# Optimization experiments

Measured on AMD Instinct MI355X. Metric: run time of the kernel, lower is better.

The kernel has to match this reference:

```python
import jax, jax.numpy as jnp
import numpy as np

N_NODES = 50000
N_EDGES = 800000
NODE_FEAT = 176
EDGE_FEAT = 4
HIDDEN = 64
LAYERS = 4
LN_EPS = 1e-5


def setup_inputs() -> dict:
    key = jax.random.key(0)
    ks = jax.random.split(key, 20)
    H, H2, Hh = HIDDEN, HIDDEN * 2, HIDDEN // 2
    inp = {
        "x": jax.random.normal(ks[0], (N_NODES, NODE_FEAT), jnp.float32),
        "edge_index": jax.random.randint(ks[1], (2, N_EDGES), 0, N_NODES, jnp.int64),
        "edge_attr": jax.random.normal(ks[2], (N_EDGES, EDGE_FEAT), jnp.float32),
        # input projection
        "in_w": jax.random.normal(ks[3], (NODE_FEAT, H), jnp.float32) * 0.05,
        "in_b": jnp.zeros((H,), jnp.float32),
        # per-layer GINEConv params (stacked over LAYERS)
        "edge_w": jax.random.normal(ks[4], (LAYERS, EDGE_FEAT, H), jnp.float32) * 0.1,
        "edge_b": jnp.zeros((LAYERS, H), jnp.float32),
        "mlp_w1": jax.random.normal(ks[5], (LAYERS, H, H2), jnp.float32) * 0.05,
        "mlp_b1": jnp.zeros((LAYERS, H2), jnp.float32),
        "mlp_w2": jax.random.normal(ks[6], (LAYERS, H2, H), jnp.float32) * 0.05,
        "mlp_b2": jnp.zeros((LAYERS, H), jnp.float32),
        "ln_g": jnp.ones((LAYERS, H), jnp.float32),
        "ln_b": jnp.zeros((LAYERS, H), jnp.float32),
        "reg_w1": jax.random.normal(ks[7], (H, Hh), jnp.float32) * 0.1,
        "reg_b1": jnp.zeros((Hh,), jnp.float32),
        "reg_w2": jax.random.normal(ks[8], (Hh, 1), jnp.float32) * 0.1,
        "reg_b2": jnp.zeros((1,), jnp.float32),
    }
    return inp


def _layernorm(z, g, b):
    mu = jnp.mean(z, axis=-1, keepdims=True)
    var = jnp.mean((z - mu) ** 2, axis=-1, keepdims=True)
    return g * (z - mu) * jax.lax.rsqrt(var + LN_EPS) + b


def reference(x, edge_index, edge_attr, in_w, in_b, edge_w, edge_b,
              mlp_w1, mlp_b1, mlp_w2, mlp_b2, ln_g, ln_b,
              reg_w1, reg_b1, reg_w2, reg_b2):
    src, dst = edge_index[0], edge_index[1]
    h = x @ in_w + in_b  # [N, H]
    for l in range(LAYERS):
        e = edge_attr @ edge_w[l] + edge_b[l]              # [E, H] edge projection
        msg = jax.nn.relu(h[src] + e)                      # gather + relu
        aggr = jax.ops.segment_sum(msg, dst, num_segments=h.shape[0])  # scatter-add
        z = h + aggr                                       # (1+eps)*x_i + aggr, eps=0
        z = jax.nn.relu(z @ mlp_w1[l] + mlp_b1[l]) @ mlp_w2[l] + mlp_b2[l]
        h = jax.nn.relu(_layernorm(z, ln_g[l], ln_b[l]))
    g = jnp.sum(h, axis=0)                                 # global_add_pool, single graph
    out = jax.nn.relu(g @ reg_w1 + reg_b1) @ reg_w2 + reg_b2
    return out.squeeze()
```

## Files before the change

### kernel.cpp

```cpp
#include <hip/hip_runtime.h>

#define N_NODES 50000
#define N_EDGES 800000
#define NODE_FEAT 176
#define HIDDEN 64
#define LN_EPS 1e-5f
#define SCAN_NB 49

typedef short bf16x8 __attribute__((ext_vector_type(8)));
typedef float f32x4 __attribute__((ext_vector_type(4)));

__device__ __forceinline__ unsigned short f2bf(float f) {
    unsigned int u = __float_as_uint(f);
    u += 0x7FFFu + ((u >> 16) & 1u);
    return (unsigned short)(u >> 16);
}
__device__ __forceinline__ int pack2(float lo, float hi) {
    return (int)(((unsigned)f2bf(hi) << 16) | (unsigned)f2bf(lo));
}
__device__ __forceinline__ float bf2f(unsigned short s) {
    return __uint_as_float(((unsigned int)s) << 16);
}
__device__ __forceinline__ float wave_sum64(float v) {
#pragma unroll
    for (int o = 32; o > 0; o >>= 1) v += __shfl_xor(v, o);
    return v;
}
__device__ __forceinline__ float sum16(float v) {
#pragma unroll
    for (int o = 8; o > 0; o >>= 1) v += __shfl_xor(v, o);
    return v;
}

__global__ __launch_bounds__(256) void k_wprep(const float* __restrict__ in_w,
                                               const float* __restrict__ w1,
                                               const float* __restrict__ w2,
                                               unsigned short* __restrict__ fin,
                                               unsigned short* __restrict__ f1,
                                               unsigned short* __restrict__ f2) {
    int t = blockIdx.x * 256 + threadIdx.x;
    if (t < 12288) {
        int e = t;
        int r = e & 7, lane = (e >> 3) & 63, j = (e >> 9) & 3, s = e >> 11;
        int k = s * 32 + ((lane >> 4) << 3) + r;
        int n = (j << 4) + (lane & 15);
        fin[e] = (k < NODE_FEAT) ? f2bf(in_w[k * 64 + n]) : (unsigned short)0;
    } else if (t < 12288 + 32768) {
        int e = t - 12288;
        int L = e >> 13, e2 = e & 8191;
        int r = e2 & 7, lane = (e2 >> 3) & 63, j = (e2 >> 9) & 7, s = (e2 >> 12) & 1;
        int k = s * 32 + ((lane >> 4) << 3) + r;
        int n = (j << 4) + (lane & 15);
        f1[e] = f2bf(w1[L * 8192 + k * 128 + n]);
    } else {
        int e = t - 45056;
        int L = e >> 13, e2 = e & 8191;
        int r = e2 & 7, lane = (e2 >> 3) & 63, j = (e2 >> 9) & 3, s = (e2 >> 11) & 3;
        int k = s * 32 + ((lane >> 4) << 3) + r;
        int n = (j << 4) + (lane & 15);
        f2[e] = f2bf(w2[L * 8192 + k * 64 + n]);
    }
}

__global__ __launch_bounds__(256) void k_inproj_mfma(const float* __restrict__ x,
                                                     const unsigned short* __restrict__ wfrag,
                                                     const float* __restrict__ in_b,
                                                     float* __restrict__ h,
                                                     unsigned short* __restrict__ hb) {
    __shared__ unsigned short lw[12288];
    const int tid = threadIdx.x;
    {
        const bf16x8* src = (const bf16x8*)wfrag;
        bf16x8* dst = (bf16x8*)lw;
        for (int i = tid; i < 1536; i += 256) dst[i] = src[i];
    }
    __syncthreads();
    const int wv = tid >> 6, lane = tid & 63;
    const int lrow = lane & 15, lgrp = lane >> 4;
    float ib[4];
#pragma unroll
    for (int j = 0; j < 4; ++j) ib[j] = in_b[16 * j + lrow];
    const int nwaves = gridDim.x * 4;
    for (int tile = blockIdx.x * 4 + wv; tile < 3125; tile += nwaves) {
        const int m0 = tile * 16;
        f32x4 acc[4];
#pragma unroll
        for (int j = 0; j < 4; ++j) acc[j] = (f32x4){ib[j], ib[j], ib[j], ib[j]};
#pragma unroll
        for (int s = 0; s < 6; ++s) {
            const int kbase = s * 32 + lgrp * 8;
            bf16x8 a;
            if (kbase < NODE_FEAT) {
                const float* p = x + (size_t)(m0 + lrow) * NODE_FEAT + kbase;
                float4 fa = *(const float4*)p;
                float4 fb = *(const float4*)(p + 4);
                a[0] = (short)f2bf(fa.x); a[1] = (short)f2bf(fa.y);
                a[2] = (short)f2bf(fa.z); a[3] = (short)f2bf(fa.w);
                a[4] = (short)f2bf(fb.x); a[5] = (short)f2bf(fb.y);
                a[6] = (short)f2bf(fb.z); a[7] = (short)f2bf(fb.w);
            } else {
                a = (bf16x8){0, 0, 0, 0, 0, 0, 0, 0};
            }
#pragma unroll
            for (int j = 0; j < 4; ++j) {
                bf16x8 b = *(const bf16x8*)&lw[((s * 4 + j) * 64 + lane) * 8];
                acc[j] = __builtin_amdgcn_mfma_f32_16x16x32_bf16(a, b, acc[j], 0, 0, 0);
            }
        }
#pragma unroll
        for (int j = 0; j < 4; ++j) {
            const int col = 16 * j + lrow;
#pragma unroll
            for (int r = 0; r < 4; ++r) {
                const int node = m0 + lgrp * 4 + r;
                float v = acc[j][r];
                h[(size_t)node * 64 + col] = v;
                hb[(size_t)node * 64 + col] = f2bf(v);
            }
        }
    }
}

__global__ __launch_bounds__(256) void k_hist(const int* __restrict__ ei,
                                              int* __restrict__ cnt,
                                              int* __restrict__ erank) {
    int e = blockIdx.x * 256 + threadIdx.x;
    if (e < N_EDGES) erank[e] = atomicAdd(&cnt[ei[N_EDGES + e]], 1);
}

__global__ __launch_bounds__(256) void k_scan_part(const int* __restrict__ cnt,
                                                   int* __restrict__ blksum) {
    const int b = blockIdx.x, t = threadIdx.x;
    const int base = b * 1024 + t * 4;
    int s = 0;
#pragma unroll
    for (int i = 0; i < 4; ++i) {
        int idx = base + i;
        if (idx < N_NODES) s += cnt[idx];
    }
#pragma unroll
    for (int o = 32; o > 0; o >>= 1) s += __shfl_xor(s, o);
    __shared__ int wt[4];
    if ((t & 63) == 0) wt[t >> 6] = s;
    __syncthreads();
    if (t == 0) blksum[b] = wt[0] + wt[1] + wt[2] + wt[3];
}

__global__ __launch_bounds__(64) void k_scan_top(const int* __restrict__ blksum,
                                                 int* __restrict__ blkoff,
                                                 int* __restrict__ row_last) {
    const int t = threadIdx.x;
    int v = (t < SCAN_NB) ? blksum[t] : 0;
    int incl = v;
#pragma unroll
    for (int o = 1; o < 64; o <<= 1) {
        int u = __shfl_up(incl, o);
        if (t >= o) incl += u;
    }
    if (t < SCAN_NB) blkoff[t] = incl - v;
    if (t == 63) row_last[0] = incl;
}

__global__ __launch_bounds__(256) void k_scan_add(const int* __restrict__ cnt,
                                                  const int* __restrict__ blkoff,
                                                  int* __restrict__ row_ptr) {
    const int b = blockIdx.x, t = threadIdx.x;
    const int base = b * 1024 + t * 4;
    int c[4];
    int tsum = 0;
#pragma unroll
    for (int i = 0; i < 4; ++i) {
        int idx = base + i;
        c[i] = (idx < N_NODES) ? cnt[idx] : 0;
        tsum += c[i];
    }
    int incl = tsum;
#pragma unroll
    for (int o = 1; o < 64; o <<= 1) {
        int u = __shfl_up(incl, o);
        if ((t & 63) >= o) incl += u;
    }
    __shared__ int wt[4];
    const int wv = t >> 6;
    if ((t & 63) == 63) wt[wv] = incl;
    __syncthreads();
    int run = blkoff[b] + (incl - tsum);
    for (int w = 0; w < wv; ++w) run += wt[w];
#pragma unroll
    for (int i = 0; i < 4; ++i) {
        int idx = base + i;
        if (idx < N_NODES) row_ptr[idx] = run;
        run += c[i];
    }
}

__global__ __launch_bounds__(256) void k_scatter(const int* __restrict__ ei,
                                                 const float4* __restrict__ ea,
                                                 const int* __restrict__ row_ptr,
                                                 const int* __restrict__ erank,
                                                 int4* __restrict__ rec) {
    int e = blockIdx.x * 256 + threadIdx.x;
    if (e >= N_EDGES) return;
    int d = ei[N_EDGES + e];
    float4 a = ea[e];
    int4 r;
    r.x = pack2(a.x, a.y);
    r.y = pack2(a.z, a.w);
    r.z = ei[e];
    r.w = 0;
    rec[row_ptr[d] + erank[e]] = r;
}

__global__ __launch_bounds__(256) void k_aggr(const float* __restrict__ h_in,
                                              const unsigned short* __restrict__ hb_in,
                                              float* __restrict__ z,
                                              const int* __restrict__ row_ptr,
                                              const int4* __restrict__ rec,
                                              const float* __restrict__ ew,
                                              const float* __restrict__ eb) {
    const int wv = threadIdx.x >> 6, lane = threadIdx.x & 63;
    const int node = blockIdx.x * 4 + wv;
    const float ew0 = ew[0 * 64 + lane], ew1 = ew[1 * 64 + lane];
    const float ew2 = ew[2 * 64 + lane], ew3 = ew[3 * 64 + lane];
    const float ebl = eb[lane];
    const int beg = __builtin_amdgcn_readfirstlane(row_ptr[node]);
    const int end = __builtin_amdgcn_readfirstlane(row_ptr[node + 1]);
    float acc = h_in[(size_t)node * 64 + lane];
    int i = beg;
    for (; i + 7 < end; i += 8) {
        int d0[8], d1[8], sx[8];
#pragma unroll
        for (int t = 0; t < 8; ++t) {
            int4 r = rec[i + t];
            d0[t] = __builtin_amdgcn_readfirstlane(r.x);
            d1[t] = __builtin_amdgcn_readfirstlane(r.y);
            sx[t] = __builtin_amdgcn_readfirstlane(r.z);
        }
        float gg[8];
#pragma unroll
        for (int t = 0; t < 8; ++t) {
            const unsigned short* __restrict__ p = hb_in + ((size_t)sx[t] << 6);
            gg[t] = bf2f(p[lane]);
        }
#pragma unroll
        for (int t = 0; t < 8; ++t) {
            float a0 = __uint_as_float((unsigned)d0[t] << 16);
            float a1 = __uint_as_float((unsigned)d0[t] & 0xffff0000u);
            float a2 = __uint_as_float((unsigned)d1[t] << 16);
            float a3 = __uint_as_float((unsigned)d1[t] & 0xffff0000u);
            float v = fmaf(a0, ew0, fmaf(a1, ew1, fmaf(a2, ew2, fmaf(a3, ew3, ebl))));
            acc += fmaxf(v + gg[t], 0.0f);
        }
    }
    for (; i < end; ++i) {
        int4 r = rec[i];
        int d0 = __builtin_amdgcn_readfirstlane(r.x);
        int d1 = __builtin_amdgcn_readfirstlane(r.y);
        int sx = __builtin_amdgcn_readfirstlane(r.z);
        const unsigned short* __restrict__ p = hb_in + ((size_t)sx << 6);
        float g0 = bf2f(p[lane]);
        float a0 = __uint_as_float((unsigned)d0 << 16);
        float a1 = __uint_as_float((unsigned)d0 & 0xffff0000u);
        float a2 = __uint_as_float((unsigned)d1 << 16);
        float a3 = __uint_as_float((unsigned)d1 & 0xffff0000u);
        float v = fmaf(a0, ew0, fmaf(a1, ew1, fmaf(a2, ew2, fmaf(a3, ew3, ebl))));
        acc += fmaxf(v + g0, 0.0f);
    }
    z[(size_t)node * 64 + lane] = acc;
}

__global__ __launch_bounds__(256) void k_mlp_mfma(float* __restrict__ z,
                                                  unsigned short* __restrict__ hb_out,
                                                  const unsigned short* __restrict__ f1,
                                                  const unsigned short* __restrict__ f2,
                                                  const float* __restrict__ b1,
                                                  const float* __restrict__ b2,
                                                  const float* __restrict__ lng,
                                                  const float* __restrict__ lnb) {
    __shared__ unsigned short w1f[8192];
    __shared__ unsigned short w2f[8192];
    __shared__ unsigned short z1s[4][2048];
    const int tid = threadIdx.x;
    {
        const bf16x8* s1 = (const bf16x8*)f1;
        const bf16x8* s2 = (const bf16x8*)f2;
        bf16x8* d1 = (bf16x8*)w1f;
        bf16x8* d2 = (bf16x8*)w2f;
        for (int i = tid; i < 1024; i += 256) { d1[i] = s1[i]; d2[i] = s2[i]; }
    }
    __syncthreads();
    const int wv = tid >> 6, lane = tid & 63;
    const int lrow = lane & 15, lgrp = lane >> 4;
    unsigned short* zs = z1s[wv];
    float bb1[8], bb2[4], g4[4], be4[4];
#pragma unroll
    for (int j = 0; j < 8; ++j) bb1[j] = b1[16 * j + lrow];
#pragma unroll
    for (int j = 0; j < 4; ++j) {
        bb2[j] = b2[16 * j + lrow];
        g4[j] = lng[16 * j + lrow];
        be4[j] = lnb[16 * j + lrow];
    }
    const int nwaves = gridDim.x * 4;
    for (int tile = blockIdx.x * 4 + wv; tile < 3125; tile += nwaves) {
        const int m0 = tile * 16;
        f32x4 acc1[8];
#pragma unroll
        for (int j = 0; j < 8; ++j) acc1[j] = (f32x4){bb1[j], bb1[j], bb1[j], bb1[j]};
#pragma unroll
        for (int s = 0; s < 2; ++s) {
            const int kbase = s * 32 + lgrp * 8;
            const float* p = z + (size_t)(m0 + lrow) * 64 + kbase;
            float4 fa = *(const float4*)p;
            float4 fb = *(const float4*)(p + 4);
            bf16x8 a;
            a[0] = (short)f2bf(fa.x); a[1] = (short)f2bf(fa.y);
            a[2] = (short)f2bf(fa.z); a[3] = (short)f2bf(fa.w);
            a[4] = (short)f2bf(fb.x); a[5] = (short)f2bf(fb.y);
            a[6] = (short)f2bf(fb.z); a[7] = (short)f2bf(fb.w);
#pragma unroll
            for (int j = 0; j < 8; ++j) {
                bf16x8 b = *(const bf16x8*)&w1f[((s * 8 + j) * 64 + lane) * 8];
                acc1[j] = __builtin_amdgcn_mfma_f32_16x16x32_bf16(a, b, acc1[j], 0, 0, 0);
            }
        }
#pragma unroll
        for (int j = 0; j < 8; ++j) {
            const int col = 16 * j + lrow;
#pragma unroll
            for (int r = 0; r < 4; ++r) {
                const int row = lgrp * 4 + r;
                const int idx = (row * 128 + col) ^ ((row & 7) << 3);
                zs[idx] = f2bf(fmaxf(acc1[j][r], 0.0f));
            }
        }
        f32x4 acc2[4];
#pragma unroll
        for (int j = 0; j < 4; ++j) acc2[j] = (f32x4){bb2[j], bb2[j], bb2[j], bb2[j]};
#pragma unroll
        for (int s = 0; s < 4; ++s) {
            const int kbase = s * 32 + lgrp * 8;
            const int idx = (lrow * 128 + kbase) ^ ((lrow & 7) << 3);
            bf16x8 a = *(const bf16x8*)&zs[idx];
#pragma unroll
            for (int j = 0; j < 4; ++j) {
                bf16x8 b = *(const bf16x8*)&w2f[((s * 4 + j) * 64 + lane) * 8];
                acc2[j] = __builtin_amdgcn_mfma_f32_16x16x32_bf16(a, b, acc2[j], 0, 0, 0);
            }
        }
#pragma unroll
        for (int r = 0; r < 4; ++r) {
            float sum = acc2[0][r] + acc2[1][r] + acc2[2][r] + acc2[3][r];
            sum = sum16(sum);
            const float mu = sum * (1.0f / 64.0f);
            float sq = 0.0f;
#pragma unroll
            for (int j = 0; j < 4; ++j) {
                float d = acc2[j][r] - mu;
                sq = fmaf(d, d, sq);
            }
            sq = sum16(sq);
            const float rstd = rsqrtf(sq * (1.0f / 64.0f) + LN_EPS);
            const int node = m0 + lgrp * 4 + r;
#pragma unroll
            for (int j = 0; j < 4; ++j) {
                const int col = 16 * j + lrow;
                float d = acc2[j][r] - mu;
                float hn = fmaxf(fmaf(g4[j] * d, rstd, be4[j]), 0.0f);
                z[(size_t)node * 64 + col] = hn;
                hb_out[(size_t)node * 64 + col] = f2bf(hn);
            }
        }
    }
}

__global__ __launch_bounds__(256) void k_pool(const float* __restrict__ h,
                                              float* __restrict__ g) {
    __shared__ float red[256];
    const int tid = threadIdx.x;
    const int lane = tid & 63;
    float part = 0.0f;
    for (int i = blockIdx.x * 4 + (tid >> 6); i < N_NODES; i += gridDim.x * 4)
        part += h[(size_t)i * 64 + lane];
    red[tid] = part;
    __syncthreads();
    if (tid < 64) {
        float s = red[tid] + red[tid + 64] + red[tid + 128] + red[tid + 192];
        atomicAdd(&g[tid], s);
    }
}

__global__ __launch_bounds__(64) void k_reg(const float* __restrict__ g,
                                            const float* __restrict__ w1,
                                            const float* __restrict__ b1,
                                            const float* __restrict__ w2,
                                            const float* __restrict__ b2,
                                            float* __restrict__ out) {
    const int j = threadIdx.x;
    const int jm = j & 31;
    float acc = b1[jm];
#pragma unroll 8
    for (int k = 0; k < 64; ++k) {
        float gk = g[k];
        acc = fmaf(gk, w1[k * 32 + jm], acc);
    }
    float contrib = (j < 32) ? fmaxf(acc, 0.0f) * w2[jm] : 0.0f;
    float s = wave_sum64(contrib);
    if (j == 0) out[0] = s + b2[0];
}

extern "C" void kernel_launch(void* const* d_in, const int* in_sizes, int n_in,
                              void* d_out, int out_size, void* d_ws, size_t ws_size,
                              hipStream_t stream) {
    const float* x      = (const float*)d_in[0];
    const int*   ei     = (const int*)d_in[1];
    const float* ea     = (const float*)d_in[2];
    const float* in_w   = (const float*)d_in[3];
    const float* in_b   = (const float*)d_in[4];
    const float* edge_w = (const float*)d_in[5];
    const float* edge_b = (const float*)d_in[6];
    const float* mlp_w1 = (const float*)d_in[7];
    const float* mlp_b1 = (const float*)d_in[8];
    const float* mlp_w2 = (const float*)d_in[9];
    const float* mlp_b2 = (const float*)d_in[10];
    const float* ln_g   = (const float*)d_in[11];
    const float* ln_b   = (const float*)d_in[12];
    const float* reg_w1 = (const float*)d_in[13];
    const float* reg_b1 = (const float*)d_in[14];
    const float* reg_w2 = (const float*)d_in[15];
    const float* reg_b2 = (const float*)d_in[16];

    char* ws = (char*)d_ws;
    float*          h0      = (float*)ws;          ws += (size_t)N_NODES * 64 * 4;
    float*          h1      = (float*)ws;          ws += (size_t)N_NODES * 64 * 4;
    int4*           rec     = (int4*)ws;           ws += (size_t)N_EDGES * 16;
    unsigned short* hb0     = (unsigned short*)ws; ws += (size_t)N_NODES * 64 * 2;
    unsigned short* hb1     = (unsigned short*)ws; ws += (size_t)N_NODES * 64 * 2;
    unsigned short* fin     = (unsigned short*)ws; ws += 12288 * 2;
    unsigned short* f1      = (unsigned short*)ws; ws += 32768 * 2;
    unsigned short* f2      = (unsigned short*)ws; ws += 32768 * 2;
    int*            erank   = (int*)ws;            ws += (size_t)N_EDGES * 4;
    int*            row_ptr = (int*)ws;            ws += (size_t)(N_NODES + 1) * 4;
    int*            cnt     = (int*)ws;            ws += (size_t)N_NODES * 4;
    int*            blksum  = (int*)ws;            ws += SCAN_NB * 4;
    int*            blkoff  = (int*)ws;            ws += SCAN_NB * 4;
    float*          g       = (float*)ws;          ws += 64 * 4;
    float*          outf    = (float*)d_out;

    const int eb_blocks = (N_EDGES + 255) / 256;

    k_wprep<<<304, 256, 0, stream>>>(in_w, mlp_w1, mlp_w2, fin, f1, f2);

    (void)hipMemsetAsync(cnt, 0, N_NODES * sizeof(int), stream);
    k_hist<<<eb_blocks, 256, 0, stream>>>(ei, cnt, erank);
    k_scan_part<<<SCAN_NB, 256, 0, stream>>>(cnt, blksum);
    k_scan_top<<<1, 64, 0, stream>>>(blksum, blkoff, row_ptr + N_NODES);
    k_scan_add<<<SCAN_NB, 256, 0, stream>>>(cnt, blkoff, row_ptr);
    k_scatter<<<eb_blocks, 256, 0, stream>>>(ei, (const float4*)ea, row_ptr, erank, rec);

    k_inproj_mfma<<<512, 256, 0, stream>>>(x, fin, in_b, h0, hb0);

    float* hA = h0;
    float* hB = h1;
    unsigned short* hbA = hb0;
    unsigned short* hbB = hb1;
    for (int l = 0; l < 4; ++l) {
        k_aggr<<<N_NODES / 4, 256, 0, stream>>>(hA, hbA, hB, row_ptr, rec,
                                                edge_w + l * 4 * 64,
                                                edge_b + l * 64);
        k_mlp_mfma<<<256, 256, 0, stream>>>(hB, hbB,
                                            f1 + l * 8192, f2 + l * 8192,
                                            mlp_b1 + l * 128, mlp_b2 + l * 64,
                                            ln_g + l * 64, ln_b + l * 64);
        float* t = hA; hA = hB; hB = t;
        unsigned short* tb = hbA; hbA = hbB; hbB = tb;
    }

    (void)hipMemsetAsync(g, 0, 64 * sizeof(float), stream);
    k_pool<<<256, 256, 0, stream>>>(hA, g);
    k_reg<<<1, 64, 0, stream>>>(g, reg_w1, reg_b1, reg_w2, reg_b2, outf);
}
```

Baseline: 287.4 us.

## Drop fp32 node buffers, keep bf16 activations; widen aggregation unroll and fold memsets

Removes the fp32 copies of h and z. The aggregation kernel now writes a bf16 z that the MLP reads directly, and the MLP and input projection write only bf16 h. The edge loop is unrolled to 16 with a masked tail, the MLP grid grows to 768 blocks, and the cnt memset moves into the weight-prep kernel. Pooling now writes per-block partials that the regressor reduces, replacing the atomics and the second memset. This cuts global memory traffic and launch count, but the residual and aggregate are now stored in bf16, which loses precision.

Result: slower. 297.3 us (+3.5%).

```diff
diff --git a/kernel.cpp b/kernel.cpp
--- a/kernel.cpp
+++ b/kernel.cpp
@@ -37,8 +37,10 @@
                                                const float* __restrict__ w2,
                                                unsigned short* __restrict__ fin,
                                                unsigned short* __restrict__ f1,
-                                               unsigned short* __restrict__ f2) {
+                                               unsigned short* __restrict__ f2,
+                                               int* __restrict__ cnt) {
     int t = blockIdx.x * 256 + threadIdx.x;
+    if (t < N_NODES) cnt[t] = 0;
     if (t < 12288) {
         int e = t;
         int r = e & 7, lane = (e >> 3) & 63, j = (e >> 9) & 3, s = e >> 11;
@@ -52,7 +54,7 @@
         int k = s * 32 + ((lane >> 4) << 3) + r;
         int n = (j << 4) + (lane & 15);
         f1[e] = f2bf(w1[L * 8192 + k * 128 + n]);
-    } else {
+    } else if (t < 12288 + 32768 + 32768) {
         int e = t - 45056;
         int L = e >> 13, e2 = e & 8191;
         int r = e2 & 7, lane = (e2 >> 3) & 63, j = (e2 >> 9) & 3, s = (e2 >> 11) & 3;
@@ -65,7 +67,6 @@
 __global__ __launch_bounds__(256) void k_inproj_mfma(const float* __restrict__ x,
                                                      const unsigned short* __restrict__ wfrag,
                                                      const float* __restrict__ in_b,
-                                                     float* __restrict__ h,
                                                      unsigned short* __restrict__ hb) {
     __shared__ unsigned short lw[12288];
     const int tid = threadIdx.x;
@@ -113,9 +114,7 @@
 #pragma unroll
             for (int r = 0; r < 4; ++r) {
                 const int node = m0 + lgrp * 4 + r;
-                float v = acc[j][r];
-                h[(size_t)node * 64 + col] = v;
-                hb[(size_t)node * 64 + col] = f2bf(v);
+                hb[(size_t)node * 64 + col] = f2bf(acc[j][r]);
             }
         }
     }
@@ -211,9 +210,8 @@
     rec[row_ptr[d] + erank[e]] = r;
 }
 
-__global__ __launch_bounds__(256) void k_aggr(const float* __restrict__ h_in,
-                                              const unsigned short* __restrict__ hb_in,
-                                              float* __restrict__ z,
+__global__ __launch_bounds__(256) void k_aggr(const unsigned short* __restrict__ hb_in,
+                                              unsigned short* __restrict__ zb,
                                               const int* __restrict__ row_ptr,
                                               const int4* __restrict__ rec,
                                               const float* __restrict__ ew,
@@ -225,25 +223,23 @@
     const float ebl = eb[lane];
     const int beg = __builtin_amdgcn_readfirstlane(row_ptr[node]);
     const int end = __builtin_amdgcn_readfirstlane(row_ptr[node + 1]);
-    float acc = h_in[(size_t)node * 64 + lane];
+    float acc = bf2f(hb_in[(size_t)node * 64 + lane]);
     int i = beg;
-    for (; i + 7 < end; i += 8) {
-        int d0[8], d1[8], sx[8];
-#pragma unroll
-        for (int t = 0; t < 8; ++t) {
+    for (; i + 16 <= end; i += 16) {
+        int d0[16], d1[16], sx[16];
+#pragma unroll
+        for (int t = 0; t < 16; ++t) {
             int4 r = rec[i + t];
             d0[t] = __builtin_amdgcn_readfirstlane(r.x);
             d1[t] = __builtin_amdgcn_readfirstlane(r.y);
             sx[t] = __builtin_amdgcn_readfirstlane(r.z);
         }
-        float gg[8];
-#pragma unroll
-        for (int t = 0; t < 8; ++t) {
-            const unsigned short* __restrict__ p = hb_in + ((size_t)sx[t] << 6);
-            gg[t] = bf2f(p[lane]);
-        }
-#pragma unroll
-        for (int t = 0; t < 8; ++t) {
+        float gg[16];
+#pragma unroll
+        for (int t = 0; t < 16; ++t)
+            gg[t] = bf2f(hb_in[((size_t)sx[t] << 6) + lane]);
+#pragma unroll
+        for (int t = 0; t < 16; ++t) {
             float a0 = __uint_as_float((unsigned)d0[t] << 16);
             float a1 = __uint_as_float((unsigned)d0[t] & 0xffff0000u);
             float a2 = __uint_as_float((unsigned)d1[t] << 16);
@@ -252,24 +248,36 @@
             acc += fmaxf(v + gg[t], 0.0f);
         }
     }
-    for (; i < end; ++i) {
-        int4 r = rec[i];
-        int d0 = __builtin_amdgcn_readfirstlane(r.x);
-        int d1 = __builtin_amdgcn_readfirstlane(r.y);
-        int sx = __builtin_amdgcn_readfirstlane(r.z);
-        const unsigned short* __restrict__ p = hb_in + ((size_t)sx << 6);
-        float g0 = bf2f(p[lane]);
-        float a0 = __uint_as_float((unsigned)d0 << 16);
-        float a1 = __uint_as_float((unsigned)d0 & 0xffff0000u);
-        float a2 = __uint_as_float((unsigned)d1 << 16);
-        float a3 = __uint_as_float((unsigned)d1 & 0xffff0000u);
-        float v = fmaf(a0, ew0, fmaf(a1, ew1, fmaf(a2, ew2, fmaf(a3, ew3, ebl))));
-        acc += fmaxf(v + g0, 0.0f);
-    }
-    z[(size_t)node * 64 + lane] = acc;
-}
-
-__global__ __launch_bounds__(256) void k_mlp_mfma(float* __restrict__ z,
+    if (i < end) {
+        const int n = end - i;
+        int d0[16], d1[16], sx[16];
+#pragma unroll
+        for (int t = 0; t < 16; ++t) {
+            int idx = i + ((t < n) ? t : (n - 1));
+            int4 r = rec[idx];
+            d0[t] = __builtin_amdgcn_readfirstlane(r.x);
+            d1[t] = __builtin_amdgcn_readfirstlane(r.y);
+            sx[t] = __builtin_amdgcn_readfirstlane(r.z);
+        }
+        float gg[16];
+#pragma unroll
+        for (int t = 0; t < 16; ++t)
+            gg[t] = bf2f(hb_in[((size_t)sx[t] << 6) + lane]);
+#pragma unroll
+        for (int t = 0; t < 16; ++t) {
+            float m = (t < n) ? 1.0f : 0.0f;
+            float a0 = __uint_as_float((unsigned)d0[t] << 16);
+            float a1 = __uint_as_float((unsigned)d0[t] & 0xffff0000u);
+            float a2 = __uint_as_float((unsigned)d1[t] << 16);
+            float a3 = __uint_as_float((unsigned)d1[t] & 0xffff0000u);
+            float v = fmaf(a0, ew0, fmaf(a1, ew1, fmaf(a2, ew2, fmaf(a3, ew3, ebl))));
+            acc += m * fmaxf(v + gg[t], 0.0f);
+        }
+    }
+    zb[(size_t)node * 64 + lane] = f2bf(acc);
+}
+
+__global__ __launch_bounds__(256) void k_mlp_mfma(const unsigned short* __restrict__ zb,
                                                   unsigned short* __restrict__ hb_out,
                                                   const unsigned short* __restrict__ f1,
                                                   const unsigned short* __restrict__ f2,
@@ -310,14 +318,7 @@
 #pragma unroll
         for (int s = 0; s < 2; ++s) {
             const int kbase = s * 32 + lgrp * 8;
-            const float* p = z + (size_t)(m0 + lrow) * 64 + kbase;
-            float4 fa = *(const float4*)p;
-            float4 fb = *(const float4*)(p + 4);
-            bf16x8 a;
-            a[0] = (short)f2bf(fa.x); a[1] = (short)f2bf(fa.y);
-            a[2] = (short)f2bf(fa.z); a[3] = (short)f2bf(fa.w);
-            a[4] = (short)f2bf(fb.x); a[5] = (short)f2bf(fb.y);
-            a[6] = (short)f2bf(fb.z); a[7] = (short)f2bf(fb.w);
+            bf16x8 a = *(const bf16x8*)&zb[(size_t)(m0 + lrow) * 64 + kbase];
 #pragma unroll
             for (int j = 0; j < 8; ++j) {
                 bf16x8 b = *(const bf16x8*)&w1f[((s * 8 + j) * 64 + lane) * 8];
@@ -367,41 +368,44 @@
                 const int col = 16 * j + lrow;
                 float d = acc2[j][r] - mu;
                 float hn = fmaxf(fmaf(g4[j] * d, rstd, be4[j]), 0.0f);
-                z[(size_t)node * 64 + col] = hn;
                 hb_out[(size_t)node * 64 + col] = f2bf(hn);
             }
         }
     }
 }
 
-__global__ __launch_bounds__(256) void k_pool(const float* __restrict__ h,
-                                              float* __restrict__ g) {
+__global__ __launch_bounds__(256) void k_pool(const unsigned short* __restrict__ hb,
+                                              float* __restrict__ gpart) {
     __shared__ float red[256];
     const int tid = threadIdx.x;
     const int lane = tid & 63;
     float part = 0.0f;
     for (int i = blockIdx.x * 4 + (tid >> 6); i < N_NODES; i += gridDim.x * 4)
-        part += h[(size_t)i * 64 + lane];
+        part += bf2f(hb[(size_t)i * 64 + lane]);
     red[tid] = part;
     __syncthreads();
     if (tid < 64) {
-        float s = red[tid] + red[tid + 64] + red[tid + 128] + red[tid + 192];
-        atomicAdd(&g[tid], s);
-    }
-}
-
-__global__ __launch_bounds__(64) void k_reg(const float* __restrict__ g,
+        gpart[blockIdx.x * 64 + tid] = red[tid] + red[tid + 64] + red[tid + 128] + red[tid + 192];
+    }
+}
+
+__global__ __launch_bounds__(64) void k_reg(const float* __restrict__ gpart,
                                             const float* __restrict__ w1,
                                             const float* __restrict__ b1,
                                             const float* __restrict__ w2,
                                             const float* __restrict__ b2,
                                             float* __restrict__ out) {
     const int j = threadIdx.x;
+    float gj = 0.0f;
+    for (int b = 0; b < 256; ++b) gj += gpart[b * 64 + j];
+    __shared__ float gs[64];
+    gs[j] = gj;
+    __syncthreads();
     const int jm = j & 31;
     float acc = b1[jm];
 #pragma unroll 8
     for (int k = 0; k < 64; ++k) {
-        float gk = g[k];
+        float gk = gs[k];
         acc = fmaf(gk, w1[k * 32 + jm], acc);
     }
     float contrib = (j < 32) ? fmaxf(acc, 0.0f) * w2[jm] : 0.0f;
@@ -431,11 +435,10 @@
     const float* reg_b2 = (const float*)d_in[16];
 
     char* ws = (char*)d_ws;
-    float*          h0      = (float*)ws;          ws += (size_t)N_NODES * 64 * 4;
-    float*          h1      = (float*)ws;          ws += (size_t)N_NODES * 64 * 4;
-    int4*           rec     = (int4*)ws;           ws += (size_t)N_EDGES * 16;
     unsigned short* hb0     = (unsigned short*)ws; ws += (size_t)N_NODES * 64 * 2;
     unsigned short* hb1     = (unsigned short*)ws; ws += (size_t)N_NODES * 64 * 2;
+    unsigned short* zb      = (unsigned short*)ws; ws += (size_t)N_NODES * 64 * 2;
+    int4*           rec     = (int4*)ws;           ws += (size_t)N_EDGES * 16;
     unsigned short* fin     = (unsigned short*)ws; ws += 12288 * 2;
     unsigned short* f1      = (unsigned short*)ws; ws += 32768 * 2;
     unsigned short* f2      = (unsigned short*)ws; ws += 32768 * 2;
@@ -444,39 +447,34 @@
     int*            cnt     = (int*)ws;            ws += (size_t)N_NODES * 4;
     int*            blksum  = (int*)ws;            ws += SCAN_NB * 4;
     int*            blkoff  = (int*)ws;            ws += SCAN_NB * 4;
-    float*          g       = (float*)ws;          ws += 64 * 4;
+    float*          gpart   = (float*)ws;          ws += 256 * 64 * 4;
     float*          outf    = (float*)d_out;
 
     const int eb_blocks = (N_EDGES + 255) / 256;
 
-    k_wprep<<<304, 256, 0, stream>>>(in_w, mlp_w1, mlp_w2, fin, f1, f2);
-
-    (void)hipMemsetAsync(cnt, 0, N_NODES * sizeof(int), stream);
+    k_wprep<<<304, 256, 0, stream>>>(in_w, mlp_w1, mlp_w2, fin, f1, f2, cnt);
+
     k_hist<<<eb_blocks, 256, 0, stream>>>(ei, cnt, erank);
     k_scan_part<<<SCAN_NB, 256, 0, stream>>>(cnt, blksum);
     k_scan_top<<<1, 64, 0, stream>>>(blksum, blkoff, row_ptr + N_NODES);
     k_scan_add<<<SCAN_NB, 256, 0, stream>>>(cnt, blkoff, row_ptr);
     k_scatter<<<eb_blocks, 256, 0, stream>>>(ei, (const float4*)ea, row_ptr, erank, rec);
 
-    k_inproj_mfma<<<512, 256, 0, stream>>>(x, fin, in_b, h0, hb0);
-
-    float* hA = h0;
-    float* hB = h1;
+    k_inproj_mfma<<<512, 256, 0, stream>>>(x, fin, in_b, hb0);
+
     unsigned short* hbA = hb0;
     unsigned short* hbB = hb1;
     for (int l = 0; l < 4; ++l) {
-        k_aggr<<<N_NODES / 4, 256, 0, stream>>>(hA, hbA, hB, row_ptr, rec,
+        k_aggr<<<N_NODES / 4, 256, 0, stream>>>(hbA, zb, row_ptr, rec,
                                                 edge_w + l * 4 * 64,
                                                 edge_b + l * 64);
-        k_mlp_mfma<<<256, 256, 0, stream>>>(hB, hbB,
+        k_mlp_mfma<<<768, 256, 0, stream>>>(zb, hbB,
                                             f1 + l * 8192, f2 + l * 8192,
                                             mlp_b1 + l * 128, mlp_b2 + l * 64,
                                             ln_g + l * 64, ln_b + l * 64);
-        float* t = hA; hA = hB; hB = t;
         unsigned short* tb = hbA; hbA = hbB; hbB = tb;
     }
 
-    (void)hipMemsetAsync(g, 0, 64 * sizeof(float), stream);
-    k_pool<<<256, 256, 0, stream>>>(hA, g);
-    k_reg<<<1, 64, 0, stream>>>(g, reg_w1, reg_b1, reg_w2, reg_b2, outf);
-}
+    k_pool<<<256, 256, 0, stream>>>(hbA, gpart);
+    k_reg<<<1, 64, 0, stream>>>(gpart, reg_w1, reg_b1, reg_w2, reg_b2, outf);
+}
```
